# Optimization experiments

Measured on AMD Instinct MI355X. Metric: run time of the kernel, lower is better.

Reference implementation:

```python
import jax, jax.numpy as jnp
import numpy as np

T, H = 2048, 1024
NH, NKV, HD = 8, 2, 128
E, TOPK, NG, TKG = 16, 4, 4, 2
F, FS = 1024, 1024
EPS = 1e-6
ROUTED_SCALE = 2.0
THETA = 10000.0


def _rmsnorm(x, w):
    return x * jax.lax.rsqrt(jnp.mean(x * x, axis=-1, keepdims=True) + EPS) * w


def setup_inputs() -> dict:
    key = jax.random.key(0)
    ks = jax.random.split(key, 12)
    s = 0.02
    return {
        "hidden_states": jax.random.normal(ks[0], (T, H), jnp.float32),
        "residual": jax.random.normal(ks[1], (T, H), jnp.float32),
        "position_ids": jnp.arange(T, dtype=jnp.int32),
        "ln1_w": jnp.ones((H,), jnp.float32),
        "qkv_w": s * jax.random.normal(ks[2], (H, (NH + 2 * NKV) * HD), jnp.float32),
        "qnorm_w": jnp.ones((HD,), jnp.float32),
        "knorm_w": jnp.ones((HD,), jnp.float32),
        "dense_w": s * jax.random.normal(ks[3], (NH * HD, H), jnp.float32),
        "ln2_w": jnp.ones((H,), jnp.float32),
        "gate_w": s * jax.random.normal(ks[4], (H, E), jnp.float32),
        "expert_bias": 0.1 * jax.random.normal(ks[5], (E,), jnp.float32),
        "w13": s * jax.random.normal(ks[6], (E, H, 2 * F), jnp.float32),
        "w2": s * jax.random.normal(ks[7], (E, F, H), jnp.float32),
        "ws_gate_up": s * jax.random.normal(ks[8], (H, 2 * FS), jnp.float32),
        "ws_down": s * jax.random.normal(ks[9], (FS, H), jnp.float32),
    }


def block_forward(hidden_states, residual, position_ids, ln1_w, qkv_w, qnorm_w,
                  knorm_w, dense_w, ln2_w, gate_w, expert_bias, w13, w2,
                  ws_gate_up, ws_down):
    # fused add + RMSNorm (input_layernorm with residual)
    resid = hidden_states + residual
    h = _rmsnorm(resid, ln1_w)

    # --- attention ---
    qkv = h @ qkv_w  # [T, (NH+2*NKV)*HD]
    q = qkv[:, : NH * HD].reshape(T, NH, HD)
    k = qkv[:, NH * HD : (NH + NKV) * HD].reshape(T, NKV, HD)
    v = qkv[:, (NH + NKV) * HD :].reshape(T, NKV, HD)
    q = _rmsnorm(q, qnorm_w)  # qk-norm per head_dim
    k = _rmsnorm(k, knorm_w)

    # neox-style RoPE over full head_dim
    inv_freq = 1.0 / (THETA ** (jnp.arange(0, HD, 2, dtype=jnp.float32) / HD))
    ang = position_ids.astype(jnp.float32)[:, None] * inv_freq[None, :]  # [T, HD/2]
    cos = jnp.cos(ang)[:, None, :]
    sin = jnp.sin(ang)[:, None, :]

    def rope(x):
        x1, x2 = x[..., : HD // 2], x[..., HD // 2 :]
        return jnp.concatenate([x1 * cos - x2 * sin, x2 * cos + x1 * sin], axis=-1)

    q, k = rope(q), rope(k)
    rep = NH // NKV
    kr = jnp.repeat(k, rep, axis=1)  # [T, NH, HD]
    vr = jnp.repeat(v, rep, axis=1)

    scores = jnp.einsum("qhd,khd->hqk", q, kr) * (HD ** -0.5)
    causal = jnp.tril(jnp.ones((T, T), bool))
    scores = jnp.where(causal[None], scores, jnp.finfo(scores.dtype).min)
    probs = jax.nn.softmax(scores, axis=-1)
    ctx = jnp.einsum("hqk,khd->qhd", probs, vr).reshape(T, NH * HD)
    attn_out = ctx @ dense_w

    # fused add + RMSNorm (post_attention_layernorm)
    resid2 = attn_out + resid
    h2 = _rmsnorm(resid2, ln2_w)

    # --- MoE router: sigmoid scoring + correction bias, grouped top-k ---
    logits = h2.astype(jnp.float32) @ gate_w  # router in fp32
    s_scores = jax.nn.sigmoid(logits)  # [T, E]
    sfc = s_scores + expert_bias[None, :]
    gview = sfc.reshape(T, NG, E // NG)
    gscores = jax.lax.top_k(gview, 2)[0].sum(-1)  # sum of top-2 per group
    gidx = jax.lax.top_k(gscores, TKG)[1]  # [T, TKG]
    gmask = jax.nn.one_hot(gidx, NG, dtype=sfc.dtype).sum(1)  # [T, NG]
    smask = jnp.repeat(gmask, E // NG, axis=1)  # [T, E]
    masked = jnp.where(smask > 0, sfc, -jnp.inf)
    topk_idx = jax.lax.top_k(masked, TOPK)[1]  # [T, TOPK]
    topk_w = jnp.take_along_axis(s_scores, topk_idx, axis=1)  # weights w/o bias
    topk_w = topk_w / (topk_w.sum(-1, keepdims=True) + 1e-20)  # renormalize
    combine = (jax.nn.one_hot(topk_idx, E, dtype=topk_w.dtype) * topk_w[..., None]).sum(1)  # [T, E]

    # routed experts (dense-over-experts reference for the grouped GEMM)
    gu = jnp.einsum("th,ehf->tef", h2, w13)  # [T, E, 2F]
    g, u = gu[..., :F], gu[..., F:]
    act = jax.nn.silu(g) * u
    y = jnp.einsum("tef,efh->teh", act, w2)
    routed = jnp.einsum("teh,te->th", y, combine) * ROUTED_SCALE

    # shared expert (SwiGLU MLP)
    su = h2 @ ws_gate_up
    shared = (jax.nn.silu(su[:, :FS]) * su[:, FS:]) @ ws_down

    mlp_out = routed + shared
    return mlp_out, resid2


def reference(hidden_states, residual, position_ids, ln1_w, qkv_w, qnorm_w,
              knorm_w, dense_w, ln2_w, gate_w, expert_bias, w13, w2,
              ws_gate_up, ws_down):
    return block_forward(hidden_states, residual, position_ids, ln1_w, qkv_w,
                         qnorm_w, knorm_w, dense_w, ln2_w, gate_w, expert_bias,
                         w13, w2, ws_gate_up, ws_down)
```

## Files before the change

### kernel.cpp

```cpp
#include <hip/hip_runtime.h>
#include <hip/hip_bf16.h>


#define T_TOK 2048
#define H_DIM 1024
#define NHEAD 8
#define NKVH 2
#define HDIM 128
#define QKV_DIM 1536
#define E_EXP 16
#define TOPKE 4
#define F_DIM 1024
#define FS_DIM 1024
#define NPAIR (T_TOK*TOPKE)
#define EPS_F 1e-6f

#define DEV __device__ __forceinline__

typedef __attribute__((ext_vector_type(4))) float f32x4;
typedef __attribute__((ext_vector_type(8))) short s16x8;

DEV float us2f(unsigned short u){ return __uint_as_float(((unsigned int)u)<<16); }
DEV unsigned short f2us(float f){
  __hip_bfloat16 b = __float2bfloat16(f);
  unsigned short u; __builtin_memcpy(&u,&b,2); return u;
}

DEV void gl2lds16(const void* g, void* l){
  __builtin_amdgcn_global_load_lds(
      (const __attribute__((address_space(1))) void*)g,
      (__attribute__((address_space(3))) void*)l, 16, 0, 0);
}

DEV float bred_sum(float v, float* sm){
  #pragma unroll
  for(int o=32;o>0;o>>=1) v += __shfl_down(v,o);
  int w = threadIdx.x>>6, l = threadIdx.x&63;
  __syncthreads();
  if(l==0) sm[w]=v;
  __syncthreads();
  return sm[0]+sm[1]+sm[2]+sm[3];
}

__global__ __launch_bounds__(256) void k_cvt_t(const float* __restrict__ in,
    unsigned short* __restrict__ out, int Kd, int Nd){
  const int z = blockIdx.z;
  const int kb = blockIdx.y*32, nb = blockIdx.x*32;
  __shared__ float Lt[32][33];
  const int tid = threadIdx.x;
  const int r = tid>>3, c4 = (tid&7)*4;
  const float* src = in + (long long)z*Kd*Nd + (long long)(kb+r)*Nd + nb + c4;
  float4 v = *(const float4*)src;
  Lt[r][c4+0]=v.x; Lt[r][c4+1]=v.y; Lt[r][c4+2]=v.z; Lt[r][c4+3]=v.w;
  __syncthreads();
  ushort4 o;
  o.x = f2us(Lt[c4+0][r]); o.y = f2us(Lt[c4+1][r]);
  o.z = f2us(Lt[c4+2][r]); o.w = f2us(Lt[c4+3][r]);
  *(ushort4*)(out + (long long)z*Nd*Kd + (long long)(nb+r)*Kd + kb + c4) = o;
}

template<bool GROUPED, bool GATHER>
__global__ __launch_bounds__(256) void gemm_mfma(
    const unsigned short* __restrict__ A, int lda,
    const unsigned short* __restrict__ Bt, int ldbt, long long bstride,
    unsigned short* __restrict__ C, int ldc,
    const int* __restrict__ rowidx, const int* __restrict__ grpoff,
    int Mdense, int K){
  const int z = blockIdx.z;
  const int rb = GROUPED ? grpoff[z] : 0;
  const int re = GROUPED ? grpoff[z+1] : Mdense;
  const int m0 = rb + blockIdx.y*128;
  if(m0 >= re) return;
  const int n0 = blockIdx.x*128;
  const unsigned short* Bz = Bt + (long long)z*bstride;

  __shared__ unsigned short As[128][32];
  __shared__ unsigned short Bs[128][32];

  const int tid = threadIdx.x;
  const int s0 = tid, s1 = tid+256;
  int gr0 = m0 + (s0>>2), gr1 = m0 + (s1>>2);
  if(GROUPED){ gr0 = min(gr0, re-1); gr1 = min(gr1, re-1); }
  if(GATHER){ gr0 = rowidx[gr0]; gr1 = rowidx[gr1]; }
  const unsigned short* ag0 = A + (long long)gr0*lda + (s0&3)*8;
  const unsigned short* ag1 = A + (long long)gr1*lda + (s1&3)*8;
  const unsigned short* bg0 = Bz + (long long)(n0 + (s0>>2))*ldbt + (s0&3)*8;
  const unsigned short* bg1 = Bz + (long long)(n0 + (s1>>2))*ldbt + (s1&3)*8;
  char* asb = (char*)&As[0][0];
  char* bsb = (char*)&Bs[0][0];
  const int wb = (tid & 192)*16;

  const int w = tid>>6, lane = tid&63;
  const int wm = (w>>1)*64, wn = (w&1)*64;
  const int fr = lane&15, q8 = (lane>>4)*8;

  f32x4 zero = {0.f,0.f,0.f,0.f};
  f32x4 acc[4][4];
  #pragma unroll
  for(int mi=0;mi<4;mi++)
    #pragma unroll
    for(int ni=0;ni<4;ni++) acc[mi][ni]=zero;

  for(int k0=0;k0<K;k0+=32){
    __syncthreads();
    gl2lds16(ag0 + k0, asb + wb);
    gl2lds16(ag1 + k0, asb + 4096 + wb);
    gl2lds16(bg0 + k0, bsb + wb);
    gl2lds16(bg1 + k0, bsb + 4096 + wb);
    __syncthreads();
    s16x8 af[4], bf[4];
    #pragma unroll
    for(int mi=0;mi<4;mi++) af[mi] = *(const s16x8*)&As[wm+mi*16+fr][q8];
    #pragma unroll
    for(int ni=0;ni<4;ni++) bf[ni] = *(const s16x8*)&Bs[wn+ni*16+fr][q8];
    #pragma unroll
    for(int mi=0;mi<4;mi++)
      #pragma unroll
      for(int ni=0;ni<4;ni++)
        acc[mi][ni] = __builtin_amdgcn_mfma_f32_16x16x32_bf16(af[mi], bf[ni], acc[mi][ni], 0,0,0);
  }
  const int q4 = (lane>>4)*4;
  #pragma unroll
  for(int mi=0;mi<4;mi++)
    #pragma unroll
    for(int ni=0;ni<4;ni++){
      const int col = n0 + wn + ni*16 + fr;
      #pragma unroll
      for(int r=0;r<4;r++){
        const int row = m0 + wm + mi*16 + q4 + r;
        if(row < re) C[(long long)row*ldc + col] = f2us(acc[mi][ni][r]);
      }
    }
}

__global__ __launch_bounds__(256) void k_silu(const unsigned short* __restrict__ gu,
    unsigned short* __restrict__ act){
  const int r = blockIdx.x, c = threadIdx.x*4;
  const ushort4 g4 = *(const ushort4*)(gu + (long long)r*2048 + c);
  const ushort4 u4 = *(const ushort4*)(gu + (long long)r*2048 + 1024 + c);
  float g[4] = {us2f(g4.x),us2f(g4.y),us2f(g4.z),us2f(g4.w)};
  float u[4] = {us2f(u4.x),us2f(u4.y),us2f(u4.z),us2f(u4.w)};
  ushort4 o;
  o.x = f2us((g[0]/(1.f+__expf(-g[0])))*u[0]);
  o.y = f2us((g[1]/(1.f+__expf(-g[1])))*u[1]);
  o.z = f2us((g[2]/(1.f+__expf(-g[2])))*u[2]);
  o.w = f2us((g[3]/(1.f+__expf(-g[3])))*u[3]);
  *(ushort4*)(act + (long long)r*1024 + c) = o;
}

__global__ __launch_bounds__(256) void k_add_rmsnorm(const float* __restrict__ hs,
    const float* __restrict__ rs, const float* __restrict__ w,
    float* __restrict__ resid, float* __restrict__ h){
  int t = blockIdx.x, tid = threadIdx.x;
  __shared__ float sm[4];
  const long base = (long)t*H_DIM;
  float x[4]; float ss = 0.f;
  #pragma unroll
  for(int i=0;i<4;i++){
    int c = tid + i*256;
    float v = hs[base+c] + rs[base+c];
    x[i]=v; resid[base+c]=v; ss += v*v;
  }
  float tot = bred_sum(ss, sm);
  float rms = rsqrtf(tot/(float)H_DIM + EPS_F);
  #pragma unroll
  for(int i=0;i<4;i++){
    int c = tid + i*256;
    h[base+c] = x[i]*rms*w[c];
  }
}

template<int EPI_ADD>
__global__ __launch_bounds__(256) void gemm_f32(
    const float* __restrict__ A, int lda,
    const float* __restrict__ B, int ldb,
    float* __restrict__ C, int ldc,
    const float* __restrict__ D, int M, int K){
  const int m0 = blockIdx.y*128;
  const int n0 = blockIdx.x*64;
  __shared__ float As[16][132];
  __shared__ float Bs[16][65];
  float acc[8][4];
  #pragma unroll
  for(int i=0;i<8;i++)
    #pragma unroll
    for(int j=0;j<4;j++) acc[i][j]=0.f;
  const int tid = threadIdx.x;
  const int tx = tid & 15, ty = tid >> 4;
  const int ar = tid >> 1, ac = (tid & 1)*8;
  const int brr = tid >> 4, bc = (tid & 15)*4;
  const float* Aptr = A + (long long)(m0+ar)*lda;
  for(int k0=0;k0<K;k0+=16){
    float4 a0 = *(const float4*)(Aptr + k0 + ac);
    float4 a1 = *(const float4*)(Aptr + k0 + ac + 4);
    float4 bv = *(const float4*)(B + (long long)(k0+brr)*ldb + n0 + bc);
    __syncthreads();
    As[ac+0][ar]=a0.x; As[ac+1][ar]=a0.y; As[ac+2][ar]=a0.z; As[ac+3][ar]=a0.w;
    As[ac+4][ar]=a1.x; As[ac+5][ar]=a1.y; As[ac+6][ar]=a1.z; As[ac+7][ar]=a1.w;
    Bs[brr][bc+0]=bv.x; Bs[brr][bc+1]=bv.y; Bs[brr][bc+2]=bv.z; Bs[brr][bc+3]=bv.w;
    __syncthreads();
    #pragma unroll
    for(int kk=0;kk<16;kk++){
      float a[8], b[4];
      #pragma unroll
      for(int i=0;i<8;i++) a[i]=As[kk][ty*8+i];
      #pragma unroll
      for(int j=0;j<4;j++) b[j]=Bs[kk][tx*4+j];
      #pragma unroll
      for(int i=0;i<8;i++)
        #pragma unroll
        for(int j=0;j<4;j++) acc[i][j] = fmaf(a[i], b[j], acc[i][j]);
    }
  }
  #pragma unroll
  for(int i=0;i<8;i++){
    int r = m0 + ty*8 + i;
    float* crow = C + (long long)r*ldc + n0 + tx*4;
    float4 v = make_float4(acc[i][0],acc[i][1],acc[i][2],acc[i][3]);
    if(EPI_ADD){
      const float4 d = *(const float4*)(D + (long long)r*ldc + n0 + tx*4);
      v.x+=d.x; v.y+=d.y; v.z+=d.z; v.w+=d.w;
    }
    *(float4*)crow = v;
  }
}

__global__ __launch_bounds__(64) void k_qkv_post(const float* __restrict__ qkv,
    const float* __restrict__ qw, const float* __restrict__ kw,
    const int* __restrict__ pos,
    float* __restrict__ qb, float* __restrict__ kb, float* __restrict__ vb){
  int slot = blockIdx.x, t = blockIdx.y, lane = threadIdx.x;
  const float* x = qkv + (long long)t*QKV_DIM + slot*HDIM;
  float x0 = x[lane], x1 = x[lane+64];
  if(slot < 10){
    float ss = x0*x0 + x1*x1;
    #pragma unroll
    for(int o=32;o>0;o>>=1) ss += __shfl_xor(ss,o);
    float rms = rsqrtf(ss/(float)HDIM + EPS_F);
    const float* w = (slot<8)? qw : kw;
    float n0 = x0*rms*w[lane];
    float n1 = x1*rms*w[lane+64];
    float p = (float)pos[t];
    float invf = __expf(-((float)lane/64.f)*9.210340371976184f);
    float ang = p*invf;
    float s = sinf(ang), c = cosf(ang);
    float o0 = n0*c - n1*s;
    float o1 = n1*c + n0*s;
    float* dst = (slot<8)? (qb + ((long long)slot*T_TOK + t)*HDIM)
                         : (kb + ((long long)(slot-8)*T_TOK + t)*HDIM);
    dst[lane]=o0; dst[lane+64]=o1;
  } else {
    float* dst = vb + ((long long)(slot-10)*T_TOK + t)*HDIM;
    dst[lane]=x0; dst[lane+64]=x1;
  }
}

#define BQ 32
#define BK 64
__global__ __launch_bounds__(256) void k_flash(const float* __restrict__ qb,
    const float* __restrict__ kb, const float* __restrict__ vb,
    float* __restrict__ ctx){
  const int h = blockIdx.x, pair = blockIdx.y;
  const int kv = h >> 2;
  const int tid = threadIdx.x;
  const int tx = tid & 15, ty = tid >> 4;
  __shared__ float Qs[HDIM][34];
  __shared__ float Ks[HDIM][68];
  __shared__ float Vs[BK][HDIM];
  __shared__ float Ps[BK][34];
  const float scale = 0.08838834764831845f;

  for(int which=0; which<2; which++){
    const int qt = which ? (63 - pair) : pair;
    const int q0 = qt * BQ;
    {
      int r = tid >> 3, cb = (tid & 7) * 16;
      const float* src = qb + ((long long)h*T_TOK + q0 + r)*HDIM + cb;
      #pragma unroll
      for(int j4=0;j4<4;j4++){
        float4 v4 = *(const float4*)(src + j4*4);
        Qs[cb+j4*4+0][r]=v4.x; Qs[cb+j4*4+1][r]=v4.y;
        Qs[cb+j4*4+2][r]=v4.z; Qs[cb+j4*4+3][r]=v4.w;
      }
    }
    float m0=-1e30f, m1=-1e30f, l0=0.f, l1=0.f;
    float O0[8], O1[8];
    #pragma unroll
    for(int j=0;j<8;j++){ O0[j]=0.f; O1[j]=0.f; }
    const int nkt = (qt>>1) + 1;
    for(int kt=0; kt<nkt; kt++){
      const int k0 = kt*BK;
      __syncthreads();
      {
        int r = tid >> 2, cb = (tid & 3) * 32;
        const float* ks = kb + ((long long)kv*T_TOK + k0 + r)*HDIM + cb;
        const float* vs = vb + ((long long)kv*T_TOK + k0 + r)*HDIM + cb;
        #pragma unroll
        for(int j4=0;j4<8;j4++){
          float4 v4 = *(const float4*)(ks + j4*4);
          Ks[cb+j4*4+0][r]=v4.x; Ks[cb+j4*4+1][r]=v4.y;
          Ks[cb+j4*4+2][r]=v4.z; Ks[cb+j4*4+3][r]=v4.w;
          *(float4*)(&Vs[r][cb+j4*4]) = *(const float4*)(vs + j4*4);
        }
      }
      __syncthreads();
      float s00=0,s01=0,s02=0,s03=0,s10=0,s11=0,s12=0,s13=0;
      const float* qsp = &Qs[0][ty*2];
      const float* ksp = &Ks[0][tx*4];
      #pragma unroll 4
      for(int kk=0;kk<HDIM;kk++){
        float2 q2 = *(const float2*)(qsp + kk*34);
        float4 k4 = *(const float4*)(ksp + kk*68);
        s00=fmaf(q2.x,k4.x,s00); s01=fmaf(q2.x,k4.y,s01);
        s02=fmaf(q2.x,k4.z,s02); s03=fmaf(q2.x,k4.w,s03);
        s10=fmaf(q2.y,k4.x,s10); s11=fmaf(q2.y,k4.y,s11);
        s12=fmaf(q2.y,k4.z,s12); s13=fmaf(q2.y,k4.w,s13);
      }
      float s[2][4] = {{s00*scale,s01*scale,s02*scale,s03*scale},
                       {s10*scale,s11*scale,s12*scale,s13*scale}};
      if(kt == nkt-1){
        #pragma unroll
        for(int qi=0;qi<2;qi++)
          #pragma unroll
          for(int ki=0;ki<4;ki++)
            if(k0 + tx*4 + ki > q0 + ty*2 + qi) s[qi][ki] = -1e30f;
      }
      float rm0 = fmaxf(fmaxf(s[0][0],s[0][1]),fmaxf(s[0][2],s[0][3]));
      float rm1 = fmaxf(fmaxf(s[1][0],s[1][1]),fmaxf(s[1][2],s[1][3]));
      #pragma unroll
      for(int o=1;o<16;o<<=1){
        rm0 = fmaxf(rm0, __shfl_xor(rm0,o));
        rm1 = fmaxf(rm1, __shfl_xor(rm1,o));
      }
      float mn0 = fmaxf(m0, rm0), mn1 = fmaxf(m1, rm1);
      float a0 = __expf(m0-mn0), a1 = __expf(m1-mn1);
      float p[2][4]; float rs0=0.f, rs1=0.f;
      #pragma unroll
      for(int ki=0;ki<4;ki++){
        p[0][ki] = __expf(s[0][ki]-mn0); rs0 += p[0][ki];
        p[1][ki] = __expf(s[1][ki]-mn1); rs1 += p[1][ki];
      }
      #pragma unroll
      for(int o=1;o<16;o<<=1){
        rs0 += __shfl_xor(rs0,o);
        rs1 += __shfl_xor(rs1,o);
      }
      l0 = l0*a0 + rs0; l1 = l1*a1 + rs1;
      m0 = mn0; m1 = mn1;
      #pragma unroll
      for(int j=0;j<8;j++){ O0[j]*=a0; O1[j]*=a1; }
      #pragma unroll
      for(int ki=0;ki<4;ki++){
        Ps[tx*4+ki][ty*2+0] = p[0][ki];
        Ps[tx*4+ki][ty*2+1] = p[1][ki];
      }
      __syncthreads();
      const float* vsp = &Vs[0][tx*8];
      const float* psp = &Ps[0][ty*2];
      #pragma unroll 2
      for(int k=0;k<BK;k++){
        float2 pf = *(const float2*)(psp + k*34);
        float4 va = *(const float4*)(vsp + k*HDIM);
        float4 vb4 = *(const float4*)(vsp + k*HDIM + 4);
        O0[0]=fmaf(pf.x,va.x,O0[0]); O0[1]=fmaf(pf.x,va.y,O0[1]);
        O0[2]=fmaf(pf.x,va.z,O0[2]); O0[3]=fmaf(pf.x,va.w,O0[3]);
        O0[4]=fmaf(pf.x,vb4.x,O0[4]); O0[5]=fmaf(pf.x,vb4.y,O0[5]);
        O0[6]=fmaf(pf.x,vb4.z,O0[6]); O0[7]=fmaf(pf.x,vb4.w,O0[7]);
        O1[0]=fmaf(pf.y,va.x,O1[0]); O1[1]=fmaf(pf.y,va.y,O1[1]);
        O1[2]=fmaf(pf.y,va.z,O1[2]); O1[3]=fmaf(pf.y,va.w,O1[3]);
        O1[4]=fmaf(pf.y,vb4.x,O1[4]); O1[5]=fmaf(pf.y,vb4.y,O1[5]);
        O1[6]=fmaf(pf.y,vb4.z,O1[6]); O1[7]=fmaf(pf.y,vb4.w,O1[7]);
      }
    }
    float inv0 = 1.f/l0, inv1 = 1.f/l1;
    float* dst0 = ctx + ((long long)(q0+ty*2))*(NHEAD*HDIM) + h*HDIM + tx*8;
    float* dst1 = dst0 + NHEAD*HDIM;
    float4 o;
    o = make_float4(O0[0]*inv0,O0[1]*inv0,O0[2]*inv0,O0[3]*inv0); *(float4*)dst0 = o;
    o = make_float4(O0[4]*inv0,O0[5]*inv0,O0[6]*inv0,O0[7]*inv0); *(float4*)(dst0+4) = o;
    o = make_float4(O1[0]*inv1,O1[1]*inv1,O1[2]*inv1,O1[3]*inv1); *(float4*)dst1 = o;
    o = make_float4(O1[4]*inv1,O1[5]*inv1,O1[6]*inv1,O1[7]*inv1); *(float4*)(dst1+4) = o;
  }
}

__global__ __launch_bounds__(256) void k_rms2(const float* __restrict__ r2,
    const float* __restrict__ w, float* __restrict__ h2f,
    unsigned short* __restrict__ h2b){
  int t = blockIdx.x, tid = threadIdx.x;
  __shared__ float sm[4];
  const long base = (long)t*H_DIM;
  float x[4]; float ss=0.f;
  #pragma unroll
  for(int i=0;i<4;i++){
    int c = tid+i*256;
    float v = r2[base+c];
    x[i]=v; ss += v*v;
  }
  float tot = bred_sum(ss, sm);
  float rms = rsqrtf(tot/(float)H_DIM + EPS_F);
  #pragma unroll
  for(int i=0;i<4;i++){
    int c = tid+i*256;
    float v = x[i]*rms*w[c];
    h2f[base+c] = v;
    h2b[base+c] = f2us(v);
  }
}

__global__ __launch_bounds__(256) void k_router(const float* __restrict__ h2,
    const float* __restrict__ gw, const float* __restrict__ eb,
    int* __restrict__ topk_idx, float* __restrict__ topk_w, int* __restrict__ counts){
  int t = blockIdx.x, tid = threadIdx.x;
  int e = tid & 15, seg = tid >> 4;
  const float* hrow = h2 + (long long)t*H_DIM;
  float part = 0.f;
  #pragma unroll 4
  for(int i=0;i<64;i++){
    int hh = seg*64 + i;
    part += hrow[hh]*gw[hh*E_EXP + e];
  }
  __shared__ float pm[16][17];
  __shared__ float sS[16], sfc[16];
  pm[seg][e] = part;
  __syncthreads();
  if(tid < 16){
    float l = 0.f;
    #pragma unroll
    for(int s=0;s<16;s++) l += pm[s][tid];
    float sg = 1.f/(1.f+expf(-l));
    sS[tid]=sg; sfc[tid]=sg+eb[tid];
  }
  __syncthreads();
  if(tid==0){
    float gs[4];
    #pragma unroll
    for(int g=0; g<4; g++){
      float m1=-1e30f, m2=-1e30f;
      for(int j=0;j<4;j++){
        float v=sfc[g*4+j];
        if(v>m1){ m2=m1; m1=v; } else if(v>m2){ m2=v; }
      }
      gs[g]=m1+m2;
    }
    int g1=0; for(int g=1;g<4;g++) if(gs[g]>gs[g1]) g1=g;
    int g2=-1; for(int g=0;g<4;g++){ if(g==g1) continue; if(g2<0||gs[g]>gs[g2]) g2=g; }
    bool taken[16];
    #pragma unroll
    for(int i=0;i<16;i++) taken[i]=false;
    int idx[4];
    for(int j=0;j<4;j++){
      int best=-1; float bv=-1e30f;
      for(int i=0;i<16;i++){
        int g=i>>2;
        if(g!=g1 && g!=g2) continue;
        if(taken[i]) continue;
        if(best<0 || sfc[i]>bv){ best=i; bv=sfc[i]; }
      }
      taken[best]=true; idx[j]=best;
    }
    float w[4]; float s=0.f;
    #pragma unroll
    for(int j=0;j<4;j++){ w[j]=sS[idx[j]]; s+=w[j]; }
    s += 1e-20f;
    #pragma unroll
    for(int j=0;j<4;j++){
      topk_idx[t*4+j]=idx[j];
      topk_w[t*4+j]=w[j]/s;
      atomicAdd(&counts[idx[j]],1);
    }
  }
}

__global__ void k_zero(int* __restrict__ counts){ if(threadIdx.x<16) counts[threadIdx.x]=0; }

__global__ void k_scan(const int* __restrict__ counts, int* __restrict__ offs, int* __restrict__ cursor){
  if(threadIdx.x==0){
    int s=0;
    for(int e2=0;e2<16;e2++){ offs[e2]=s; cursor[e2]=s; s+=counts[e2]; }
    offs[16]=s;
  }
}

__global__ __launch_bounds__(256) void k_scatter(const int* __restrict__ topk_idx,
    int* __restrict__ cursor, int* __restrict__ pair_tok, int* __restrict__ tok2pair){
  int i = blockIdx.x*256 + threadIdx.x;
  int e = topk_idx[i];
  int pos = atomicAdd(&cursor[e],1);
  pair_tok[pos] = i>>2;
  tok2pair[i] = pos;
}

__global__ __launch_bounds__(256) void k_combine(const unsigned short* __restrict__ y,
    const unsigned short* __restrict__ sout, const int* __restrict__ tok2pair,
    const float* __restrict__ topk_w, float* __restrict__ out0){
  int t = blockIdx.x, tid = threadIdx.x;
  int p[4]; float w[4];
  #pragma unroll
  for(int j=0;j<4;j++){ p[j]=tok2pair[t*4+j]; w[j]=topk_w[t*4+j]*2.0f; }
  const long base = (long)t*H_DIM;
  #pragma unroll
  for(int i=0;i<4;i++){
    int c = tid + i*256;
    float v = us2f(sout[base+c]);
    #pragma unroll
    for(int j=0;j<4;j++) v += w[j]*us2f(y[(long long)p[j]*H_DIM + c]);
    out0[base+c] = v;
  }
}

extern "C" void kernel_launch(void* const* d_in, const int* in_sizes, int n_in,
                              void* d_out, int out_size, void* d_ws, size_t ws_size,
                              hipStream_t stream) {
  const float* hs   = (const float*)d_in[0];
  const float* rsd  = (const float*)d_in[1];
  const int*   pos  = (const int*)d_in[2];
  const float* ln1  = (const float*)d_in[3];
  const float* qkvw = (const float*)d_in[4];
  const float* qnw  = (const float*)d_in[5];
  const float* knw  = (const float*)d_in[6];
  const float* dw   = (const float*)d_in[7];
  const float* ln2  = (const float*)d_in[8];
  const float* gw   = (const float*)d_in[9];
  const float* eb   = (const float*)d_in[10];
  const float* w13  = (const float*)d_in[11];
  const float* w2   = (const float*)d_in[12];
  const float* wsgu = (const float*)d_in[13];
  const float* wsd  = (const float*)d_in[14];
  float* out0 = (float*)d_out;
  float* out1 = out0 + (size_t)T_TOK*H_DIM;

  char* W = (char*)d_ws;
  float* resid = (float*)(W + 0);
  float* h     = (float*)(W + 8388608);
  float* ctx   = h;
  float* qkv   = (float*)(W + 16777216);
  float* qb    = (float*)(W + 29360128);
  float* h2f   = (float*)(W + 37748736);
  float* kb    = (float*)(W + 46137344);
  float* vb    = (float*)(W + 48234496);
  unsigned short* gu    = (unsigned short*)(W + 8388608);
  unsigned short* ybuf  = (unsigned short*)(W + 8388608);
  unsigned short* sgu   = (unsigned short*)(W + 16777216);
  unsigned short* sact  = (unsigned short*)(W + 0);
  unsigned short* sout  = (unsigned short*)(W + 46137344);
  unsigned short* h2b   = (unsigned short*)(W + 50331648);
  unsigned short* act   = (unsigned short*)(W + 54525952);
  unsigned short* w13t  = (unsigned short*)(W + 71303168);
  unsigned short* w2t   = (unsigned short*)(W + 138412032);
  unsigned short* wsgut = (unsigned short*)(W + 171966464);
  unsigned short* wsdt  = (unsigned short*)(W + 176160768);
  float* topkw = (float*)(W + 178257920);
  int* topki   = (int*)(W + 178290688);
  int* ptok    = (int*)(W + 178323456);
  int* t2p     = (int*)(W + 178356224);
  int* cnt     = (int*)(W + 178388992);
  int* offs    = (int*)(W + 178389056);
  int* cur     = (int*)(W + 178389184);

  k_cvt_t<<<dim3(64,32,16), 256, 0, stream>>>(w13,  w13t,  1024, 2048);
  k_cvt_t<<<dim3(32,32,16), 256, 0, stream>>>(w2,   w2t,   1024, 1024);
  k_cvt_t<<<dim3(64,32,1),  256, 0, stream>>>(wsgu, wsgut, 1024, 2048);
  k_cvt_t<<<dim3(32,32,1),  256, 0, stream>>>(wsd,  wsdt,  1024, 1024);
  k_add_rmsnorm<<<T_TOK, 256, 0, stream>>>(hs, rsd, ln1, resid, h);
  gemm_f32<0><<<dim3(QKV_DIM/64, T_TOK/128), 256, 0, stream>>>(
      h, H_DIM, qkvw, QKV_DIM, qkv, QKV_DIM, nullptr, T_TOK, H_DIM);
  k_qkv_post<<<dim3(12, T_TOK), 64, 0, stream>>>(qkv, qnw, knw, pos, qb, kb, vb);
  k_flash<<<dim3(NHEAD, T_TOK/BQ/2), 256, 0, stream>>>(qb, kb, vb, ctx);
  gemm_f32<1><<<dim3(H_DIM/64, T_TOK/128), 256, 0, stream>>>(
      ctx, NHEAD*HDIM, dw, H_DIM, out1, H_DIM, resid, T_TOK, NHEAD*HDIM);
  k_rms2<<<T_TOK, 256, 0, stream>>>(out1, ln2, h2f, h2b);
  k_zero<<<1, 64, 0, stream>>>(cnt);
  k_router<<<T_TOK, 256, 0, stream>>>(h2f, gw, eb, topki, topkw, cnt);
  k_scan<<<1, 64, 0, stream>>>(cnt, offs, cur);
  k_scatter<<<NPAIR/256, 256, 0, stream>>>(topki, cur, ptok, t2p);
  gemm_mfma<false,false><<<dim3(16,16,1), 256, 0, stream>>>(
      h2b, 1024, wsgut, 1024, 0, sgu, 2048, nullptr, nullptr, T_TOK, 1024);
  k_silu<<<T_TOK, 256, 0, stream>>>(sgu, sact);
  gemm_mfma<false,false><<<dim3(8,16,1), 256, 0, stream>>>(
      sact, 1024, wsdt, 1024, 0, sout, 1024, nullptr, nullptr, T_TOK, 1024);
  gemm_mfma<true,true><<<dim3(16,64,16), 256, 0, stream>>>(
      h2b, 1024, w13t, 1024, (long long)2048*1024, gu, 2048, ptok, offs, 0, 1024);
  k_silu<<<NPAIR, 256, 0, stream>>>(gu, act);
  gemm_mfma<true,false><<<dim3(8,64,16), 256, 0, stream>>>(
      act, 1024, w2t, 1024, (long long)1024*1024, ybuf, 1024, nullptr, offs, 0, 1024);
  k_combine<<<T_TOK, 256, 0, stream>>>(ybuf, sout, t2p, topkw, out0);
}
```

Measured before the change: 1.170 ms.

## Split flash-attention query tiles across blocks and shuffle P via registers

The causal flash kernel now launches one block per query tile (64 blocks per head), with the heaviest tiles scheduled first, instead of pairing two tiles per block. The P matrix is broadcast through wave shuffles rather than written to shared memory, which removes one barrier and the Ps buffer. The unpadded shared arrays, a coalesced V load, a launch-bounds occupancy hint and a new output column mapping are also added. The intent is to raise parallelism and occupancy on the attention stage. In exchange, per-block load becomes uneven and the unpadded K/Q tiles may cause shared-memory bank conflicts.

```diff
diff --git a/kernel.cpp b/kernel.cpp
--- a/kernel.cpp
+++ b/kernel.cpp
@@ -255,132 +255,144 @@
   }
 }
 
-#define BQ 32
-#define BK 64
-__global__ __launch_bounds__(256) void k_flash(const float* __restrict__ qb,
+#define FBQ 32
+#define FBK 64
+__global__ __launch_bounds__(256,2) void k_flash(const float* __restrict__ qb,
     const float* __restrict__ kb, const float* __restrict__ vb,
     float* __restrict__ ctx){
-  const int h = blockIdx.x, pair = blockIdx.y;
+  const int h = blockIdx.x;
+  const int by = blockIdx.y;
+  const int qt = (by < 32) ? (63 - by) : (by - 32);
   const int kv = h >> 2;
+  const int q0 = qt * FBQ;
   const int tid = threadIdx.x;
   const int tx = tid & 15, ty = tid >> 4;
-  __shared__ float Qs[HDIM][34];
-  __shared__ float Ks[HDIM][68];
-  __shared__ float Vs[BK][HDIM];
-  __shared__ float Ps[BK][34];
+  __shared__ float Qs[HDIM][32];
+  __shared__ float Ks[HDIM][64];
+  __shared__ float Vs[FBK][HDIM];
   const float scale = 0.08838834764831845f;
 
-  for(int which=0; which<2; which++){
-    const int qt = which ? (63 - pair) : pair;
-    const int q0 = qt * BQ;
+  {
+    int r = tid>>3, cb = (tid&7)*16;
+    const float* src = qb + ((long long)h*T_TOK + q0 + r)*HDIM + cb;
+    #pragma unroll
+    for(int j=0;j<4;j++){
+      float4 v4 = *(const float4*)(src + j*4);
+      Qs[cb+j*4+0][r]=v4.x; Qs[cb+j*4+1][r]=v4.y;
+      Qs[cb+j*4+2][r]=v4.z; Qs[cb+j*4+3][r]=v4.w;
+    }
+  }
+
+  float m0=-1e30f, m1=-1e30f, l0=0.f, l1=0.f;
+  float O0[8], O1[8];
+  #pragma unroll
+  for(int j=0;j<8;j++){ O0[j]=0.f; O1[j]=0.f; }
+
+  const int nkt = (qt>>1) + 1;
+  const float* kbase = kb + (long long)kv*T_TOK*HDIM;
+  const float* vbase = vb + (long long)kv*T_TOK*HDIM;
+  const int lbase = tid & 48;
+
+  for(int kt=0; kt<nkt; kt++){
+    const int k0 = kt*FBK;
+    __syncthreads();
     {
-      int r = tid >> 3, cb = (tid & 7) * 16;
-      const float* src = qb + ((long long)h*T_TOK + q0 + r)*HDIM + cb;
-      #pragma unroll
-      for(int j4=0;j4<4;j4++){
-        float4 v4 = *(const float4*)(src + j4*4);
-        Qs[cb+j4*4+0][r]=v4.x; Qs[cb+j4*4+1][r]=v4.y;
-        Qs[cb+j4*4+2][r]=v4.z; Qs[cb+j4*4+3][r]=v4.w;
-      }
-    }
-    float m0=-1e30f, m1=-1e30f, l0=0.f, l1=0.f;
-    float O0[8], O1[8];
-    #pragma unroll
-    for(int j=0;j<8;j++){ O0[j]=0.f; O1[j]=0.f; }
-    const int nkt = (qt>>1) + 1;
-    for(int kt=0; kt<nkt; kt++){
-      const int k0 = kt*BK;
-      __syncthreads();
-      {
-        int r = tid >> 2, cb = (tid & 3) * 32;
-        const float* ks = kb + ((long long)kv*T_TOK + k0 + r)*HDIM + cb;
-        const float* vs = vb + ((long long)kv*T_TOK + k0 + r)*HDIM + cb;
-        #pragma unroll
-        for(int j4=0;j4<8;j4++){
-          float4 v4 = *(const float4*)(ks + j4*4);
-          Ks[cb+j4*4+0][r]=v4.x; Ks[cb+j4*4+1][r]=v4.y;
-          Ks[cb+j4*4+2][r]=v4.z; Ks[cb+j4*4+3][r]=v4.w;
-          *(float4*)(&Vs[r][cb+j4*4]) = *(const float4*)(vs + j4*4);
-        }
-      }
-      __syncthreads();
-      float s00=0,s01=0,s02=0,s03=0,s10=0,s11=0,s12=0,s13=0;
-      const float* qsp = &Qs[0][ty*2];
-      const float* ksp = &Ks[0][tx*4];
-      #pragma unroll 4
-      for(int kk=0;kk<HDIM;kk++){
-        float2 q2 = *(const float2*)(qsp + kk*34);
-        float4 k4 = *(const float4*)(ksp + kk*68);
-        s00=fmaf(q2.x,k4.x,s00); s01=fmaf(q2.x,k4.y,s01);
-        s02=fmaf(q2.x,k4.z,s02); s03=fmaf(q2.x,k4.w,s03);
-        s10=fmaf(q2.y,k4.x,s10); s11=fmaf(q2.y,k4.y,s11);
-        s12=fmaf(q2.y,k4.z,s12); s13=fmaf(q2.y,k4.w,s13);
-      }
-      float s[2][4] = {{s00*scale,s01*scale,s02*scale,s03*scale},
-                       {s10*scale,s11*scale,s12*scale,s13*scale}};
-      if(kt == nkt-1){
-        #pragma unroll
-        for(int qi=0;qi<2;qi++)
-          #pragma unroll
-          for(int ki=0;ki<4;ki++)
-            if(k0 + tx*4 + ki > q0 + ty*2 + qi) s[qi][ki] = -1e30f;
-      }
-      float rm0 = fmaxf(fmaxf(s[0][0],s[0][1]),fmaxf(s[0][2],s[0][3]));
-      float rm1 = fmaxf(fmaxf(s[1][0],s[1][1]),fmaxf(s[1][2],s[1][3]));
-      #pragma unroll
-      for(int o=1;o<16;o<<=1){
-        rm0 = fmaxf(rm0, __shfl_xor(rm0,o));
-        rm1 = fmaxf(rm1, __shfl_xor(rm1,o));
-      }
-      float mn0 = fmaxf(m0, rm0), mn1 = fmaxf(m1, rm1);
-      float a0 = __expf(m0-mn0), a1 = __expf(m1-mn1);
-      float p[2][4]; float rs0=0.f, rs1=0.f;
+      int r = tid>>2, cb = (tid&3)*32;
+      const float* ks = kbase + (long long)(k0+r)*HDIM + cb;
+      #pragma unroll
+      for(int j=0;j<8;j++){
+        float4 v4 = *(const float4*)(ks + j*4);
+        Ks[cb+j*4+0][r]=v4.x; Ks[cb+j*4+1][r]=v4.y;
+        Ks[cb+j*4+2][r]=v4.z; Ks[cb+j*4+3][r]=v4.w;
+      }
+      #pragma unroll
+      for(int j=0;j<8;j++){
+        int idx = tid + 256*j;
+        int vr = idx>>5, dc = (idx&31)*4;
+        *(float4*)&Vs[vr][dc] = *(const float4*)(vbase + (long long)(k0+vr)*HDIM + dc);
+      }
+    }
+    __syncthreads();
+
+    float s00=0,s01=0,s02=0,s03=0, s10=0,s11=0,s12=0,s13=0;
+    const float* qsp = &Qs[0][ty*2];
+    const float* ksp = &Ks[0][tx*4];
+    #pragma unroll 8
+    for(int kk=0;kk<HDIM;kk++){
+      float2 q2 = *(const float2*)(qsp + kk*32);
+      float4 k4 = *(const float4*)(ksp + kk*64);
+      s00=fmaf(q2.x,k4.x,s00); s01=fmaf(q2.x,k4.y,s01);
+      s02=fmaf(q2.x,k4.z,s02); s03=fmaf(q2.x,k4.w,s03);
+      s10=fmaf(q2.y,k4.x,s10); s11=fmaf(q2.y,k4.y,s11);
+      s12=fmaf(q2.y,k4.z,s12); s13=fmaf(q2.y,k4.w,s13);
+    }
+    float p0[4] = {s00*scale, s01*scale, s02*scale, s03*scale};
+    float p1[4] = {s10*scale, s11*scale, s12*scale, s13*scale};
+    if(kt == nkt-1){
+      #pragma unroll
+      for(int ci=0;ci<4;ci++){
+        int c = k0 + tx*4 + ci;
+        if(c > q0 + ty*2)     p0[ci] = -1e30f;
+        if(c > q0 + ty*2 + 1) p1[ci] = -1e30f;
+      }
+    }
+    float rm0 = fmaxf(fmaxf(p0[0],p0[1]),fmaxf(p0[2],p0[3]));
+    float rm1 = fmaxf(fmaxf(p1[0],p1[1]),fmaxf(p1[2],p1[3]));
+    #pragma unroll
+    for(int o=1;o<16;o<<=1){
+      rm0 = fmaxf(rm0, __shfl_xor(rm0,o));
+      rm1 = fmaxf(rm1, __shfl_xor(rm1,o));
+    }
+    float mn0 = fmaxf(m0,rm0), mn1 = fmaxf(m1,rm1);
+    float a0 = __expf(m0-mn0), a1 = __expf(m1-mn1);
+    float rs0=0.f, rs1=0.f;
+    #pragma unroll
+    for(int ci=0;ci<4;ci++){
+      p0[ci] = __expf(p0[ci]-mn0); rs0 += p0[ci];
+      p1[ci] = __expf(p1[ci]-mn1); rs1 += p1[ci];
+    }
+    #pragma unroll
+    for(int o=1;o<16;o<<=1){
+      rs0 += __shfl_xor(rs0,o);
+      rs1 += __shfl_xor(rs1,o);
+    }
+    l0 = l0*a0 + rs0; l1 = l1*a1 + rs1;
+    m0 = mn0; m1 = mn1;
+    #pragma unroll
+    for(int j=0;j<8;j++){ O0[j]*=a0; O1[j]*=a1; }
+
+    #pragma unroll 4
+    for(int kc=0;kc<16;kc++){
+      float pa[4], pb[4];
       #pragma unroll
       for(int ki=0;ki<4;ki++){
-        p[0][ki] = __expf(s[0][ki]-mn0); rs0 += p[0][ki];
-        p[1][ki] = __expf(s[1][ki]-mn1); rs1 += p[1][ki];
-      }
-      #pragma unroll
-      for(int o=1;o<16;o<<=1){
-        rs0 += __shfl_xor(rs0,o);
-        rs1 += __shfl_xor(rs1,o);
-      }
-      l0 = l0*a0 + rs0; l1 = l1*a1 + rs1;
-      m0 = mn0; m1 = mn1;
-      #pragma unroll
-      for(int j=0;j<8;j++){ O0[j]*=a0; O1[j]*=a1; }
+        pa[ki] = __shfl(p0[ki], lbase + kc);
+        pb[ki] = __shfl(p1[ki], lbase + kc);
+      }
       #pragma unroll
       for(int ki=0;ki<4;ki++){
-        Ps[tx*4+ki][ty*2+0] = p[0][ki];
-        Ps[tx*4+ki][ty*2+1] = p[1][ki];
-      }
-      __syncthreads();
-      const float* vsp = &Vs[0][tx*8];
-      const float* psp = &Ps[0][ty*2];
-      #pragma unroll 2
-      for(int k=0;k<BK;k++){
-        float2 pf = *(const float2*)(psp + k*34);
-        float4 va = *(const float4*)(vsp + k*HDIM);
-        float4 vb4 = *(const float4*)(vsp + k*HDIM + 4);
-        O0[0]=fmaf(pf.x,va.x,O0[0]); O0[1]=fmaf(pf.x,va.y,O0[1]);
-        O0[2]=fmaf(pf.x,va.z,O0[2]); O0[3]=fmaf(pf.x,va.w,O0[3]);
-        O0[4]=fmaf(pf.x,vb4.x,O0[4]); O0[5]=fmaf(pf.x,vb4.y,O0[5]);
-        O0[6]=fmaf(pf.x,vb4.z,O0[6]); O0[7]=fmaf(pf.x,vb4.w,O0[7]);
-        O1[0]=fmaf(pf.y,va.x,O1[0]); O1[1]=fmaf(pf.y,va.y,O1[1]);
-        O1[2]=fmaf(pf.y,va.z,O1[2]); O1[3]=fmaf(pf.y,va.w,O1[3]);
-        O1[4]=fmaf(pf.y,vb4.x,O1[4]); O1[5]=fmaf(pf.y,vb4.y,O1[5]);
-        O1[6]=fmaf(pf.y,vb4.z,O1[6]); O1[7]=fmaf(pf.y,vb4.w,O1[7]);
-      }
-    }
-    float inv0 = 1.f/l0, inv1 = 1.f/l1;
-    float* dst0 = ctx + ((long long)(q0+ty*2))*(NHEAD*HDIM) + h*HDIM + tx*8;
-    float* dst1 = dst0 + NHEAD*HDIM;
-    float4 o;
-    o = make_float4(O0[0]*inv0,O0[1]*inv0,O0[2]*inv0,O0[3]*inv0); *(float4*)dst0 = o;
-    o = make_float4(O0[4]*inv0,O0[5]*inv0,O0[6]*inv0,O0[7]*inv0); *(float4*)(dst0+4) = o;
-    o = make_float4(O1[0]*inv1,O1[1]*inv1,O1[2]*inv1,O1[3]*inv1); *(float4*)dst1 = o;
-    o = make_float4(O1[4]*inv1,O1[5]*inv1,O1[6]*inv1,O1[7]*inv1); *(float4*)(dst1+4) = o;
-  }
+        const float* vrow = &Vs[kc*4+ki][0];
+        float4 va  = *(const float4*)(vrow + tx*4);
+        float4 vb4 = *(const float4*)(vrow + 64 + tx*4);
+        float qa = pa[ki], qb2 = pb[ki];
+        O0[0]=fmaf(qa,va.x,O0[0]);  O0[1]=fmaf(qa,va.y,O0[1]);
+        O0[2]=fmaf(qa,va.z,O0[2]);  O0[3]=fmaf(qa,va.w,O0[3]);
+        O0[4]=fmaf(qa,vb4.x,O0[4]); O0[5]=fmaf(qa,vb4.y,O0[5]);
+        O0[6]=fmaf(qa,vb4.z,O0[6]); O0[7]=fmaf(qa,vb4.w,O0[7]);
+        O1[0]=fmaf(qb2,va.x,O1[0]);  O1[1]=fmaf(qb2,va.y,O1[1]);
+        O1[2]=fmaf(qb2,va.z,O1[2]);  O1[3]=fmaf(qb2,va.w,O1[3]);
+        O1[4]=fmaf(qb2,vb4.x,O1[4]); O1[5]=fmaf(qb2,vb4.y,O1[5]);
+        O1[6]=fmaf(qb2,vb4.z,O1[6]); O1[7]=fmaf(qb2,vb4.w,O1[7]);
+      }
+    }
+  }
+  float inv0 = 1.f/l0, inv1 = 1.f/l1;
+  float* dst0 = ctx + (long long)(q0 + ty*2)*(NHEAD*HDIM) + h*HDIM + tx*4;
+  float* dst1 = dst0 + NHEAD*HDIM;
+  *(float4*)dst0      = make_float4(O0[0]*inv0,O0[1]*inv0,O0[2]*inv0,O0[3]*inv0);
+  *(float4*)(dst0+64) = make_float4(O0[4]*inv0,O0[5]*inv0,O0[6]*inv0,O0[7]*inv0);
+  *(float4*)dst1      = make_float4(O1[0]*inv1,O1[1]*inv1,O1[2]*inv1,O1[3]*inv1);
+  *(float4*)(dst1+64) = make_float4(O1[4]*inv1,O1[5]*inv1,O1[6]*inv1,O1[7]*inv1);
 }
 
 __global__ __launch_bounds__(256) void k_rms2(const float* __restrict__ r2,
@@ -565,7 +577,7 @@
   gemm_f32<0><<<dim3(QKV_DIM/64, T_TOK/128), 256, 0, stream>>>(
       h, H_DIM, qkvw, QKV_DIM, qkv, QKV_DIM, nullptr, T_TOK, H_DIM);
   k_qkv_post<<<dim3(12, T_TOK), 64, 0, stream>>>(qkv, qnw, knw, pos, qb, kb, vb);
-  k_flash<<<dim3(NHEAD, T_TOK/BQ/2), 256, 0, stream>>>(qb, kb, vb, ctx);
+  k_flash<<<dim3(NHEAD, 64), 256, 0, stream>>>(qb, kb, vb, ctx);
   gemm_f32<1><<<dim3(H_DIM/64, T_TOK/128), 256, 0, stream>>>(
       ctx, NHEAD*HDIM, dw, H_DIM, out1, H_DIM, resid, T_TOK, NHEAD*HDIM);
   k_rms2<<<T_TOK, 256, 0, stream>>>(out1, ln2, h2f, h2b);
```

New measurement: 1.107 ms. 5.3% less time.
